# Optimization experiments

Hardware: AMD Instinct MI355X
Metric: run time of the kernel (lower is better)

The kernel has to match this reference:

```python
import jax, jax.numpy as jnp
import numpy as np

B = 256          # batchSize
KNEG = 4096      # K negatives
D = 128          # inputSize
N = 1000000      # outputSize (memory bank rows)
T = 0.07
MOM = 0.5
STDV = 1.0 / np.sqrt(D / 3.0)


def setup_inputs() -> dict:
    key = jax.random.key(0)
    k1, k2, k3, k4, k5, k6 = jax.random.split(key, 6)
    ab = jax.random.normal(k1, (B, D), dtype=jnp.float32)
    l = jax.random.normal(k2, (B, D), dtype=jnp.float32)
    ss = jax.random.normal(k3, (B, D), dtype=jnp.float32)
    # memory bank initialized uniform in [-stdv, stdv] like the torch buffer
    memory_ab = jax.random.uniform(k4, (N, D), dtype=jnp.float32) * (2 * STDV) - STDV
    idx = jax.random.randint(k5, (B, KNEG + 1), 0, N)
    y = jax.random.randint(k6, (B,), 0, N)
    idx = idx.at[:, 0].set(y)  # positive sample in column 0
    return {"ab": ab, "l": l, "ss": ss, "memory_ab": memory_ab,
            "idx": idx, "y": y}


def reference(ab, l, ss, memory_ab, idx, y):
    # gather: [B, K+1, D]; detached in the original (no grad to the bank)
    w = jax.lax.stop_gradient(memory_ab[idx])
    # three batched dot-product scores against the same gathered weights
    out_l = jnp.einsum('bkd,bd->bk', w, l)[..., None] / T
    out_ss = jnp.einsum('bkd,bd->bk', w, ss)[..., None] / T
    out_orig = jnp.einsum('bkd,bd->bk', w, ab)[..., None] / T
    out = jnp.stack([out_orig, out_l, out_ss])  # [3, B, K+1, 1]
    # momentum scatter-update of the memory bank (no_grad in original)
    ab_pos = memory_ab[y] * MOM + ab * (1.0 - MOM)
    ab_norm = jnp.sqrt(jnp.sum(ab_pos * ab_pos, axis=1, keepdims=True))
    new_memory_ab = jax.lax.stop_gradient(memory_ab.at[y].set(ab_pos / ab_norm))
    return out, new_memory_ab
```

## Files before the change

kernel.cpp:

```cpp
#include <hip/hip_runtime.h>
#include <math.h>

constexpr int Bc   = 256;
constexpr int KP1  = 4097;
constexpr int Dc   = 128;
constexpr int NROW = 1000000;
constexpr float MOM = 0.5f;
constexpr float Tc  = 0.07f;

typedef float f4 __attribute__((ext_vector_type(4)));

__global__ __launch_bounds__(256) void copy_mem_kernel(const f4* __restrict__ src,
                                                       f4* __restrict__ dst,
                                                       int n4) {
    int i = blockIdx.x * 256 + threadIdx.x;
    const int S = gridDim.x * 256;
    for (; i + 3 * S < n4; i += 4 * S) {
        f4 a0 = src[i];
        f4 a1 = src[i + S];
        f4 a2 = src[i + 2 * S];
        f4 a3 = src[i + 3 * S];
        __builtin_nontemporal_store(a0, &dst[i]);
        __builtin_nontemporal_store(a1, &dst[i + S]);
        __builtin_nontemporal_store(a2, &dst[i + 2 * S]);
        __builtin_nontemporal_store(a3, &dst[i + 3 * S]);
    }
    for (; i < n4; i += S) __builtin_nontemporal_store(src[i], &dst[i]);
}

__global__ __launch_bounds__(64) void scatter_kernel(const float* __restrict__ memory,
                                                     const float* __restrict__ ab,
                                                     const int* __restrict__ y,
                                                     float* __restrict__ out_mem) {
    const int b = blockIdx.x;
    const int row = y[b];
    for (int b2 = b + 1; b2 < Bc; ++b2)
        if (y[b2] == row) return;

    const int lane = threadIdx.x;
    float2 m = *(const float2*)(memory + (size_t)row * Dc + lane * 2);
    float2 a = *(const float2*)(ab + b * Dc + lane * 2);
    float v0 = m.x * MOM + a.x * (1.0f - MOM);
    float v1 = m.y * MOM + a.y * (1.0f - MOM);
    float s = v0 * v0 + v1 * v1;
#pragma unroll
    for (int off = 32; off; off >>= 1) s += __shfl_xor(s, off);
    const float inv = 1.0f / sqrtf(s);
    float2 o;
    o.x = v0 * inv;
    o.y = v1 * inv;
    *(float2*)(out_mem + (size_t)row * Dc + lane * 2) = o;
}

constexpr int GY    = 32;
constexpr int NW    = GY * 4;
constexpr int KSTEP = NW * 8;
constexpr int NITER = (KP1 + KSTEP - 1) / KSTEP;

__global__ __launch_bounds__(256) void gather_dot_kernel(
    const float* __restrict__ memory,
    const float* __restrict__ ab,
    const float* __restrict__ l,
    const float* __restrict__ ss,
    const int* __restrict__ idx,
    float* __restrict__ out) {
    const int b    = blockIdx.x;
    const int lane = threadIdx.x & 63;
    const int wid  = (threadIdx.x >> 6) + (blockIdx.y << 2);
    const int g    = lane >> 3;
    const int sub  = lane & 7;

    float4 qa[4], ql[4], qs[4];
#pragma unroll
    for (int it = 0; it < 4; ++it) {
        const int d = it * 32 + sub * 4;
        qa[it] = *(const float4*)(ab + b * Dc + d);
        ql[it] = *(const float4*)(l  + b * Dc + d);
        qs[it] = *(const float4*)(ss + b * Dc + d);
    }
    const int* idxb = idx + (size_t)b * KP1;
    const size_t out_b = (size_t)b * KP1;
    const size_t plane = (size_t)Bc * KP1;
    const float invT = 1.0f / Tc;
    const int kbase = wid * 8 + g;

    int rows[NITER];
#pragma unroll
    for (int t = 0; t < NITER; ++t) {
        int k = kbase + t * KSTEP;
        rows[t] = idxb[(k < KP1) ? k : (KP1 - 1)];
    }

#pragma unroll
    for (int t = 0; t < NITER; ++t) {
        const int k = kbase + t * KSTEP;
        const float* wrow = memory + (size_t)rows[t] * Dc;
        float sa = 0.f, sl = 0.f, s2 = 0.f;
#pragma unroll
        for (int it = 0; it < 4; ++it) {
            const float4 w = *(const float4*)(wrow + it * 32 + sub * 4);
            sa += w.x * qa[it].x + w.y * qa[it].y + w.z * qa[it].z + w.w * qa[it].w;
            sl += w.x * ql[it].x + w.y * ql[it].y + w.z * ql[it].z + w.w * ql[it].w;
            s2 += w.x * qs[it].x + w.y * qs[it].y + w.z * qs[it].z + w.w * qs[it].w;
        }
#pragma unroll
        for (int off = 1; off < 8; off <<= 1) {
            sa += __shfl_xor(sa, off);
            sl += __shfl_xor(sl, off);
            s2 += __shfl_xor(s2, off);
        }
        if (sub == 0 && k < KP1) {
            out[0 * plane + out_b + k] = sa * invT;
            out[1 * plane + out_b + k] = sl * invT;
            out[2 * plane + out_b + k] = s2 * invT;
        }
    }
}

extern "C" void kernel_launch(void* const* d_in, const int* in_sizes, int n_in,
                              void* d_out, int out_size, void* d_ws, size_t ws_size,
                              hipStream_t stream) {
    const float* ab     = (const float*)d_in[0];
    const float* l      = (const float*)d_in[1];
    const float* ss     = (const float*)d_in[2];
    const float* memory = (const float*)d_in[3];
    const int*   idx    = (const int*)d_in[4];
    const int*   y      = (const int*)d_in[5];

    float* out     = (float*)d_out;
    float* out_mem = out + (size_t)3 * Bc * KP1;

    const int n4 = (NROW * Dc) / 4;
    copy_mem_kernel<<<dim3(4096), dim3(256), 0, stream>>>(
        (const f4*)memory, (f4*)out_mem, n4);
    scatter_kernel<<<dim3(Bc), dim3(64), 0, stream>>>(memory, ab, y, out_mem);
    gather_dot_kernel<<<dim3(Bc, GY), dim3(256), 0, stream>>>(memory, ab, l, ss, idx, out);
}
```

Before: 303.9 us.

## Bucket gather indices by memory row region to improve locality

Adds a pre-pass that bins all B*(K+1) gather indices by row>>10 into workspace buckets with atomics, plus an overflow list. A new kernel then processes each bucket, so gathered rows from the same region of the bank are read together and hit cache. The aim is to cut scattered DRAM traffic from the random gather. In exchange it adds atomic build cost, extra workspace traffic, per-entry query reloads and extra launches. It also adds an overflow path, and falls back to the old path if the workspace is too small.

```diff
diff --git a/kernel.cpp b/kernel.cpp
--- a/kernel.cpp
+++ b/kernel.cpp
@@ -8,7 +8,46 @@
 constexpr float MOM = 0.5f;
 constexpr float Tc  = 0.07f;
 
+constexpr int NB    = (NROW + 1023) >> 10;
+constexpr int CAPB  = 1280;
+constexpr int OVCAP = 8192;
+
+constexpr size_t ENT_WORDS = (size_t)NB * CAPB;
+constexpr size_t OFF_CNT   = ENT_WORDS * 2;
+constexpr size_t OFF_OVCNT = OFF_CNT + NB;
+constexpr size_t OFF_OV    = OFF_OVCNT + 1;
+constexpr size_t WS_NEEDED = (OFF_OV + OVCAP) * sizeof(int);
+
 typedef float f4 __attribute__((ext_vector_type(4)));
+
+__global__ __launch_bounds__(1024) void zero_kernel(int* __restrict__ p, int n) {
+    const int i = threadIdx.x;
+    if (i < n) p[i] = 0;
+}
+
+__global__ __launch_bounds__(256) void build_kernel(const int* __restrict__ idx,
+                                                    unsigned long long* __restrict__ entries,
+                                                    int* __restrict__ cnt,
+                                                    int* __restrict__ ovcnt,
+                                                    int* __restrict__ ov) {
+    int i = blockIdx.x * 256 + threadIdx.x;
+    const int total = Bc * KP1;
+    const int S = gridDim.x * 256;
+    for (; i < total; i += S) {
+        const int row = idx[i];
+        const int bkt = row >> 10;
+        const int c = atomicAdd(&cnt[bkt], 1);
+        if (c < CAPB) {
+            const int b = i / KP1;
+            const int k = i - b * KP1;
+            entries[(size_t)bkt * CAPB + c] =
+                ((unsigned long long)row << 21) | (unsigned)((b << 13) | k);
+        } else {
+            const int o = atomicAdd(ovcnt, 1);
+            if (o < OVCAP) ov[o] = i;
+        }
+    }
+}
 
 __global__ __launch_bounds__(256) void copy_mem_kernel(const f4* __restrict__ src,
                                                        f4* __restrict__ dst,
@@ -52,6 +91,101 @@
     *(float2*)(out_mem + (size_t)row * Dc + lane * 2) = o;
 }
 
+__global__ __launch_bounds__(256) void bucket_gather_kernel(
+    const float* __restrict__ memory,
+    const float* __restrict__ ab,
+    const float* __restrict__ l,
+    const float* __restrict__ ss,
+    const int* __restrict__ cnt,
+    const unsigned long long* __restrict__ entries,
+    float* __restrict__ out) {
+    const int bkt  = blockIdx.x >> 1;
+    const int half = blockIdx.x & 1;
+    int n = cnt[bkt];
+    if (n > CAPB) n = CAPB;
+    const unsigned long long* eb = entries + (size_t)bkt * CAPB;
+    const int grp = threadIdx.x >> 3;
+    const int sub = threadIdx.x & 7;
+    const size_t plane = (size_t)Bc * KP1;
+    const float invT = 1.0f / Tc;
+
+    for (int e0 = half * 32; e0 < n; e0 += 64) {
+        const int e = e0 + grp;
+        if (e < n) {
+            const unsigned long long v = eb[e];
+            const int row = (int)(v >> 21);
+            const int bq  = (int)((v >> 13) & 255);
+            const int k   = (int)(v & 8191);
+            const float* wrow = memory + (size_t)row * Dc;
+            const float* pa = ab + bq * Dc;
+            const float* pl = l  + bq * Dc;
+            const float* ps = ss + bq * Dc;
+            float sa = 0.f, sl = 0.f, s2 = 0.f;
+#pragma unroll
+            for (int it = 0; it < 4; ++it) {
+                const int d = it * 32 + sub * 4;
+                const float4 w  = *(const float4*)(wrow + d);
+                const float4 qa = *(const float4*)(pa + d);
+                const float4 ql = *(const float4*)(pl + d);
+                const float4 qs = *(const float4*)(ps + d);
+                sa += w.x * qa.x + w.y * qa.y + w.z * qa.z + w.w * qa.w;
+                sl += w.x * ql.x + w.y * ql.y + w.z * ql.z + w.w * ql.w;
+                s2 += w.x * qs.x + w.y * qs.y + w.z * qs.z + w.w * qs.w;
+            }
+#pragma unroll
+            for (int off = 1; off < 8; off <<= 1) {
+                sa += __shfl_xor(sa, off);
+                sl += __shfl_xor(sl, off);
+                s2 += __shfl_xor(s2, off);
+            }
+            if (sub == 0) {
+                const size_t ob = (size_t)bq * KP1 + k;
+                out[0 * plane + ob] = sa * invT;
+                out[1 * plane + ob] = sl * invT;
+                out[2 * plane + ob] = s2 * invT;
+            }
+        }
+    }
+}
+
+__global__ __launch_bounds__(64) void overflow_kernel(
+    const float* __restrict__ memory,
+    const float* __restrict__ ab, const float* __restrict__ l,
+    const float* __restrict__ ss, const int* __restrict__ idx,
+    const int* __restrict__ ovcnt, const int* __restrict__ ov,
+    float* __restrict__ out) {
+    int n = *ovcnt;
+    if (n > OVCAP) n = OVCAP;
+    const int lane = threadIdx.x;
+    const size_t plane = (size_t)Bc * KP1;
+    const float invT = 1.0f / Tc;
+    for (int t = blockIdx.x; t < n; t += gridDim.x) {
+        const int i = ov[t];
+        const int b = i / KP1;
+        const int k = i - b * KP1;
+        const int row = idx[i];
+        const float2 w  = *(const float2*)(memory + (size_t)row * Dc + lane * 2);
+        const float2 qa = *(const float2*)(ab + b * Dc + lane * 2);
+        const float2 ql = *(const float2*)(l  + b * Dc + lane * 2);
+        const float2 qs = *(const float2*)(ss + b * Dc + lane * 2);
+        float sa = w.x * qa.x + w.y * qa.y;
+        float sl = w.x * ql.x + w.y * ql.y;
+        float s2 = w.x * qs.x + w.y * qs.y;
+#pragma unroll
+        for (int o = 32; o; o >>= 1) {
+            sa += __shfl_xor(sa, o);
+            sl += __shfl_xor(sl, o);
+            s2 += __shfl_xor(s2, o);
+        }
+        if (lane == 0) {
+            const size_t ob = (size_t)b * KP1 + k;
+            out[0 * plane + ob] = sa * invT;
+            out[1 * plane + ob] = sl * invT;
+            out[2 * plane + ob] = s2 * invT;
+        }
+    }
+}
+
 constexpr int GY    = 32;
 constexpr int NW    = GY * 4;
 constexpr int KSTEP = NW * 8;
@@ -90,7 +224,6 @@
         int k = kbase + t * KSTEP;
         rows[t] = idxb[(k < KP1) ? k : (KP1 - 1)];
     }
-
 #pragma unroll
     for (int t = 0; t < NITER; ++t) {
         const int k = kbase + t * KSTEP;
@@ -129,10 +262,28 @@
 
     float* out     = (float*)d_out;
     float* out_mem = out + (size_t)3 * Bc * KP1;
-
     const int n4 = (NROW * Dc) / 4;
-    copy_mem_kernel<<<dim3(4096), dim3(256), 0, stream>>>(
-        (const f4*)memory, (f4*)out_mem, n4);
-    scatter_kernel<<<dim3(Bc), dim3(64), 0, stream>>>(memory, ab, y, out_mem);
-    gather_dot_kernel<<<dim3(Bc, GY), dim3(256), 0, stream>>>(memory, ab, l, ss, idx, out);
-}
+
+    if (ws_size >= WS_NEEDED) {
+        unsigned long long* entries = (unsigned long long*)d_ws;
+        int* wsi   = (int*)d_ws;
+        int* cnt   = wsi + OFF_CNT;
+        int* ovcnt = wsi + OFF_OVCNT;
+        int* ov    = wsi + OFF_OV;
+
+        zero_kernel<<<dim3(1), dim3(1024), 0, stream>>>(cnt, NB + 1);
+        build_kernel<<<dim3(512), dim3(256), 0, stream>>>(idx, entries, cnt, ovcnt, ov);
+        copy_mem_kernel<<<dim3(4096), dim3(256), 0, stream>>>(
+            (const f4*)memory, (f4*)out_mem, n4);
+        scatter_kernel<<<dim3(Bc), dim3(64), 0, stream>>>(memory, ab, y, out_mem);
+        bucket_gather_kernel<<<dim3(2 * NB), dim3(256), 0, stream>>>(
+            memory, ab, l, ss, cnt, entries, out);
+        overflow_kernel<<<dim3(32), dim3(64), 0, stream>>>(
+            memory, ab, l, ss, idx, ovcnt, ov, out);
+    } else {
+        copy_mem_kernel<<<dim3(4096), dim3(256), 0, stream>>>(
+            (const f4*)memory, (f4*)out_mem, n4);
+        scatter_kernel<<<dim3(Bc), dim3(64), 0, stream>>>(memory, ab, y, out_mem);
+        gather_dot_kernel<<<dim3(Bc, GY), dim3(256), 0, stream>>>(memory, ab, l, ss, idx, out);
+    }
+}
```

Result: slower. 666.3 us (+119.2%).
